# Kernel optimization log

Hardware: AMD Instinct MI355X
Metric: run time of the kernel (lower is better)

## Reference

```python
import jax, jax.numpy as jnp
import numpy as np

N = 100000   # nodes
E = 800000   # edges
G = 64       # graphs in batch
H_LSTM = 256


def setup_inputs() -> dict:
    key = jax.random.key(0)
    ks = jax.random.split(key, 24)

    def rn(k, shape, scale=0.05):
        return jax.random.normal(k, shape, dtype=jnp.float32) * scale

    inp = {
        "x": jax.random.normal(ks[0], (N, 32), dtype=jnp.float32),
        "edge_index": jax.random.randint(ks[1], (2, E), 0, N, dtype=jnp.int64),
        "batch_idx": jnp.sort(jax.random.randint(ks[2], (N,), 0, G, dtype=jnp.int64)),
        # GCN layer weights (in_dim x out_dim) + bias
        "W1": rn(ks[3], (32, 128)),   "b1": jnp.zeros((128,), jnp.float32),
        "W2": rn(ks[4], (128, 256)),  "b2": jnp.zeros((256,), jnp.float32),
        "W3": rn(ks[5], (256, 512)),  "b3": jnp.zeros((512,), jnp.float32),
        # LSTM layer 0: input 512 -> hidden 256, gates order (i,f,g,o)
        "Wih0": rn(ks[6], (4 * H_LSTM, 512)), "Whh0": rn(ks[7], (4 * H_LSTM, H_LSTM)),
        "bih0": jnp.zeros((4 * H_LSTM,), jnp.float32), "bhh0": jnp.zeros((4 * H_LSTM,), jnp.float32),
        # LSTM layer 1: input 256 -> hidden 256
        "Wih1": rn(ks[8], (4 * H_LSTM, H_LSTM)), "Whh1": rn(ks[9], (4 * H_LSTM, H_LSTM)),
        "bih1": jnp.zeros((4 * H_LSTM,), jnp.float32), "bhh1": jnp.zeros((4 * H_LSTM,), jnp.float32),
        # output projection 256 -> 512
        "Wp": rn(ks[10], (512, H_LSTM)), "bp": jnp.zeros((512,), jnp.float32),
    }
    return inp


def _lstm_cell(xt, Wih, Whh, bih, bhh):
    B = xt.shape[0]
    H = Whh.shape[1]
    h0 = jnp.zeros((B, H), xt.dtype)
    c0 = jnp.zeros((B, H), xt.dtype)
    gates = xt @ Wih.T + h0 @ Whh.T + bih + bhh  # [B, 4H]
    i = jax.nn.sigmoid(gates[:, 0 * H:1 * H])
    f = jax.nn.sigmoid(gates[:, 1 * H:2 * H])
    g = jnp.tanh(gates[:, 2 * H:3 * H])
    o = jax.nn.sigmoid(gates[:, 3 * H:4 * H])
    c = f * c0 + i * g
    return o * jnp.tanh(c)


def reference(x, edge_index, batch_idx, W1, b1, W2, b2, W3, b3,
              Wih0, Whh0, bih0, bhh0, Wih1, Whh1, bih1, bhh1, Wp, bp):
    src, dst = edge_index[0], edge_index[1]
    # symmetric GCN normalization with self-loops (PyG GCNConv default)
    deg = jax.ops.segment_sum(jnp.ones((E,), x.dtype), dst, num_segments=N) + 1.0
    dinv = jax.lax.rsqrt(deg)
    edge_norm = (dinv[src] * dinv[dst])[:, None]
    self_norm = (dinv * dinv)[:, None]

    def gcn(h, W, b):
        h = h @ W                                            # transform first (smaller gather)
        msg = h[src] * edge_norm                             # [E, out]
        agg = jax.ops.segment_sum(msg, dst, num_segments=N)  # scatter-add to targets
        agg = agg + h * self_norm                            # self-loop contribution
        return jax.nn.relu(agg + b)

    h = gcn(x, W1, b1)
    h = gcn(h, W2, b2)
    h = gcn(h, W3, b3)  # [N, 512]

    # global mean pool per graph
    counts = jax.ops.segment_sum(jnp.ones((N,), h.dtype), batch_idx, num_segments=G)
    pooled = jax.ops.segment_sum(h, batch_idx, num_segments=G) / jnp.maximum(counts, 1.0)[:, None]

    # 2-layer LSTM over seq_len=1 (zero initial state)
    h1 = _lstm_cell(pooled, Wih0, Whh0, bih0, bhh0)
    h2 = _lstm_cell(h1, Wih1, Whh1, bih1, bhh1)
    return h2 @ Wp.T + bp  # [G, 512]
```

## Files before the change

kernel.cpp:

```cpp
#include <hip/hip_runtime.h>
#include <math.h>
#include <type_traits>


__device__ __forceinline__ float bf2f(unsigned short u) {
    union { unsigned int i; float f; } v; v.i = ((unsigned int)u) << 16; return v.f;
}
__device__ __forceinline__ unsigned short f2bf(float f) {
    union { float f_; unsigned int i; } v; v.f_ = f;
    unsigned int x = v.i;
    return (unsigned short)((x + 0x7fffu + ((x >> 16) & 1u)) >> 16);
}
__device__ __forceinline__ float sigm(float x) { return 1.f / (1.f + expf(-x)); }

typedef __attribute__((ext_vector_type(8))) short short8;
typedef __attribute__((ext_vector_type(16))) float f32x16;


__global__ void k_init(int* __restrict__ indeg, int* __restrict__ cursor,
                       int* __restrict__ gstart, int* __restrict__ gend,
                       float* __restrict__ pooled, int N) {
    int i = blockIdx.x * 256 + threadIdx.x;
    if (i < N) indeg[i] = 0;
    else if (i < 2 * N) cursor[i - N] = 0;
    else if (i < 2 * N + 64) gstart[i - 2 * N] = 0;
    else if (i < 2 * N + 128) gend[i - 2 * N - 64] = 0;
    else if (i < 2 * N + 128 + 64 * 512) pooled[i - 2 * N - 128] = 0.f;
}


template <int K, int NC>
__device__ __forceinline__ void prep_elem(const float* __restrict__ W,
                                          unsigned short* __restrict__ Wf, int idx) {
    constexpr int S = K / 16;
    int lane = idx & 63;
    int ts = idx >> 6;
    int s = ts % S, t = ts / S;
    int n = t * 32 + (lane & 31);
    int kb = s * 16 + (lane >> 5) * 8;
    short8 o;
    #pragma unroll
    for (int j = 0; j < 8; ++j) o[j] = (short)f2bf(W[(size_t)(kb + j) * NC + n]);
    *(short8*)(Wf + (size_t)idx * 8) = o;
}

__global__ void k_count(const int* __restrict__ dst, int* __restrict__ indeg, int E,
                        const float* __restrict__ W1, unsigned short* __restrict__ Wf1,
                        const float* __restrict__ W2, unsigned short* __restrict__ Wf2,
                        const float* __restrict__ W3, unsigned short* __restrict__ Wf3) {
    constexpr int P1 = 32 * 128 / 8, P2 = 128 * 256 / 8, P3 = 256 * 512 / 8;
    int i = blockIdx.x * 256 + threadIdx.x;
    if (i < E) atomicAdd(&indeg[dst[i]], 1);
    if (i < P1) prep_elem<32, 128>(W1, Wf1, i);
    else if (i < P1 + P2) prep_elem<128, 256>(W2, Wf2, i - P1);
    else if (i < P1 + P2 + P3) prep_elem<256, 512>(W3, Wf3, i - P1 - P2);
}


__global__ __launch_bounds__(1024) void k_scan1(const int* __restrict__ in, int* __restrict__ out,
                                                int* __restrict__ bsum, float* __restrict__ dinv,
                                                const float* __restrict__ x, float* __restrict__ xs,
                                                int N) {
    __shared__ int sd[1024];
    __shared__ float sdv[1024];
    int tid = threadIdx.x;
    int i = blockIdx.x * 1024 + tid;
    int v = (i < N) ? in[i] : 0;
    float dv = rsqrtf((float)v + 1.0f);
    if (i < N) dinv[i] = dv;
    sdv[tid] = dv;
    sd[tid] = v;
    __syncthreads();
    for (int s = 1; s < 1024; s <<= 1) {
        int t = (tid >= s) ? sd[tid - s] : 0;
        __syncthreads();
        sd[tid] += t;
        __syncthreads();
    }
    if (i < N) out[i] = sd[tid] - v;
    if (tid == 1023) bsum[blockIdx.x] = sd[1023];
    int base = blockIdx.x * 1024;
    const float4* x4 = (const float4*)x;
    float4* xs4 = (float4*)xs;
    #pragma unroll
    for (int rep = 0; rep < 8; ++rep) {
        int j = rep * 1024 + tid;
        int node = base + (j >> 3);
        if (node < N) {
            float4 t = x4[(size_t)base * 8 + j];
            float s = sdv[j >> 3];
            t.x *= s; t.y *= s; t.z *= s; t.w *= s;
            xs4[(size_t)base * 8 + j] = t;
        }
    }
}

__global__ __launch_bounds__(256) void k_scan2(int* __restrict__ bsum, int nb) {
    __shared__ int sd[256];
    int tid = threadIdx.x;
    int v = (tid < nb) ? bsum[tid] : 0;
    sd[tid] = v;
    __syncthreads();
    for (int s = 1; s < 256; s <<= 1) {
        int t = (tid >= s) ? sd[tid - s] : 0;
        __syncthreads();
        sd[tid] += t;
        __syncthreads();
    }
    if (tid < nb) bsum[tid] = sd[tid] - v;
    if (tid == 0) bsum[nb] = sd[255];
}

__global__ __launch_bounds__(1024) void k_scan3(int* __restrict__ off, const int* __restrict__ bsum,
                                                const int* __restrict__ batch,
                                                int* __restrict__ gstart, int* __restrict__ gend,
                                                int N, int nb) {
    int i = blockIdx.x * 1024 + threadIdx.x;
    if (i < N) {
        off[i] += bsum[i >> 10];
        int g = batch[i];
        if (i == 0 || batch[i - 1] != g) gstart[g] = i;
        if (i == N - 1 || batch[i + 1] != g) gend[g] = i + 1;
    } else if (i == N) {
        off[N] = bsum[nb];
    }
}

__global__ void k_fill(const int* __restrict__ src, const int* __restrict__ dst,
                       const int* __restrict__ off, int* __restrict__ cursor,
                       int* __restrict__ csrc, int E) {
    int i = blockIdx.x * 256 + threadIdx.x;
    if (i >= E) return;
    int d = dst[i];
    int p = off[d] + atomicAdd(&cursor[d], 1);
    csrc[p] = src[i];
}


template <int F, typename T>
__device__ __forceinline__ void agg_body(
        const T* __restrict__ Hin, const float* __restrict__ dinv,
        const int* __restrict__ off, const int* __restrict__ csrc,
        unsigned short* __restrict__ out, int N) {
    constexpr int R = (F >= 256) ? 4 : (F >= 128 ? 2 : 1);
    int wave = (int)((blockIdx.x * 256u + threadIdx.x) >> 6);
    int lane = threadIdx.x & 63;
    if (wave >= N) return;
    int fb = (F >= 64) ? lane * R : lane;
    bool act = fb < F;
    int s0 = off[wave], s1 = off[wave + 1];
    int L = s1 - s0;
    float corr = 1.0f - (float)(((L + 7) & ~7) - L);
    float dn = dinv[wave];
    float acc[R];
    #pragma unroll
    for (int j = 0; j < R; ++j) acc[j] = 0.f;

    for (int e = s0; e < s1; e += 8) {
        int idx[8];
        #pragma unroll
        for (int j = 0; j < 8; ++j) {
            int ee = e + j;
            int ix = csrc[ee];
            idx[j] = (ee < s1) ? ix : wave;
        }
        if (act) {
            if constexpr (std::is_same_v<T, float>) {
                float d0[8];
                #pragma unroll
                for (int j = 0; j < 8; ++j) d0[j] = Hin[(size_t)idx[j] * F + fb];
                #pragma unroll
                for (int j = 0; j < 8; ++j) acc[0] += d0[j];
            } else if constexpr (R == 4) {
                ushort4 d0[8];
                #pragma unroll
                for (int j = 0; j < 8; ++j)
                    d0[j] = *(const ushort4*)(Hin + (size_t)idx[j] * F + fb);
                #pragma unroll
                for (int j = 0; j < 8; ++j) {
                    acc[0] += bf2f(d0[j].x); acc[1] += bf2f(d0[j].y);
                    acc[2] += bf2f(d0[j].z); acc[3] += bf2f(d0[j].w);
                }
            } else {
                ushort2 d0[8];
                #pragma unroll
                for (int j = 0; j < 8; ++j)
                    d0[j] = *(const ushort2*)(Hin + (size_t)idx[j] * F + fb);
                #pragma unroll
                for (int j = 0; j < 8; ++j) {
                    acc[0] += bf2f(d0[j].x); acc[1] += bf2f(d0[j].y);
                }
            }
        }
    }
    if (act) {
        const T* ps = Hin + (size_t)wave * F + fb;
        unsigned short* pd = out + (size_t)wave * F + fb;
        if constexpr (std::is_same_v<T, float>) {
            pd[0] = f2bf((acc[0] + corr * ps[0]) * dn);
        } else if constexpr (R == 4) {
            ushort4 hv = *(const ushort4*)ps;
            ushort4 o;
            o.x = f2bf((acc[0] + corr * bf2f(hv.x)) * dn);
            o.y = f2bf((acc[1] + corr * bf2f(hv.y)) * dn);
            o.z = f2bf((acc[2] + corr * bf2f(hv.z)) * dn);
            o.w = f2bf((acc[3] + corr * bf2f(hv.w)) * dn);
            *(ushort4*)pd = o;
        } else {
            ushort2 hv = *(const ushort2*)ps;
            ushort2 o;
            o.x = f2bf((acc[0] + corr * bf2f(hv.x)) * dn);
            o.y = f2bf((acc[1] + corr * bf2f(hv.y)) * dn);
            *(ushort2*)pd = o;
        }
    }
}

__global__ __launch_bounds__(256) void k_aggL1(
        const float* __restrict__ Hin, const float* __restrict__ dinv,
        const int* __restrict__ off, const int* __restrict__ csrc,
        unsigned short* __restrict__ out, int N) {
    agg_body<32, float>(Hin, dinv, off, csrc, out, N);
}

__global__ __launch_bounds__(256) void k_aggL2(
        const unsigned short* __restrict__ Hin, const float* __restrict__ dinv,
        const int* __restrict__ off, const int* __restrict__ csrc,
        unsigned short* __restrict__ out, int N) {
    agg_body<128, unsigned short>(Hin, dinv, off, csrc, out, N);
}

__global__ __launch_bounds__(256) void k_aggL3pair(
        const unsigned short* __restrict__ Hin, const float* __restrict__ dinv,
        const int* __restrict__ off, const int* __restrict__ csrc,
        unsigned short* __restrict__ out, int N) {
    constexpr int F = 256;
    int wave = (int)((blockIdx.x * 256u + threadIdx.x) >> 6);
    int lane = threadIdx.x & 63;
    if (wave >= N) return;
    int half = lane >> 5;
    int fb = (lane & 31) * 8;
    int s0 = off[wave], s1 = off[wave + 1];
    int L = s1 - s0;
    float corrTot = 1.0f - (float)(((L + 15) & ~15) - L);
    float acc[8];
    #pragma unroll
    for (int k = 0; k < 8; ++k) acc[k] = 0.f;

    for (int e = s0; e < s1; e += 16) {
        int idx[8];
        #pragma unroll
        for (int j = 0; j < 8; ++j) {
            int ee = e + j * 2 + half;
            int ix = csrc[ee];
            idx[j] = (ee < s1) ? ix : wave;
        }
        short8 d0[8];
        #pragma unroll
        for (int j = 0; j < 8; ++j)
            d0[j] = *(const short8*)(Hin + (size_t)idx[j] * F + fb);
        #pragma unroll
        for (int j = 0; j < 8; ++j) {
            #pragma unroll
            for (int k = 0; k < 8; ++k)
                acc[k] += bf2f((unsigned short)d0[j][k]);
        }
    }
    #pragma unroll
    for (int k = 0; k < 8; ++k) acc[k] += __shfl_xor(acc[k], 32, 64);

    if (half == 0) {
        float dn = dinv[wave];
        short8 selfv = *(const short8*)(Hin + (size_t)wave * F + fb);
        short8 o;
        #pragma unroll
        for (int k = 0; k < 8; ++k)
            o[k] = (short)f2bf((acc[k] + corrTot * bf2f((unsigned short)selfv[k])) * dn);
        *(short8*)(out + (size_t)wave * F + fb) = o;
    }
}


template <int K, int NC, int POOL>
__device__ __forceinline__ void gemm_body(
        const unsigned short* __restrict__ A, const unsigned short* __restrict__ Wf,
        const float* __restrict__ bias, const float* __restrict__ dinv,
        unsigned short* __restrict__ C,
        float* __restrict__ pooled, float* __restrict__ partial,
        int* __restrict__ gtile, const int* __restrict__ batch, int M) {
    constexpr int S = K / 16;
    constexpr int CPR = K / 8;
    constexpr int NT = NC / 32;
    __shared__ unsigned short sA[64 * K];
    __shared__ int sbat[POOL ? 64 : 1];
    __shared__ float sdv[POOL ? 1 : 64];
    int tid = threadIdx.x, lane = tid & 63, w = tid >> 6;
    int q = lane >> 5, m = lane & 31;
    int row0 = blockIdx.x * 64;

    if (tid < 64) {
        int rr = row0 + tid; if (rr > M - 1) rr = M - 1;
        if (POOL) sbat[tid] = batch[rr];
        else      sdv[tid] = dinv[rr];
    }

    #pragma unroll
    for (int i = 0; i < (64 * CPR) / 256; ++i) {
        int g = i * 256 + tid;
        int mm = g / CPR, kc = g % CPR;
        int grow = row0 + mm; if (grow > M - 1) grow = M - 1;
        short8 v = *(const short8*)(A + (size_t)grow * K + kc * 8);
        int xm = (CPR >= 8) ? (mm & 7) : ((mm >> 1) & 3);
        *(short8*)(sA + (size_t)(mm * CPR + (kc ^ xm)) * 8) = v;
    }
    __syncthreads();

    int gmin = 0; bool fast = false;
    unsigned int selMask = 0;
    if (POOL) {
        gmin = sbat[0];
        fast = (sbat[63] - gmin) <= 1;
        if (tid == 0) gtile[blockIdx.x] = gmin;
        #pragma unroll
        for (int half = 0; half < 2; ++half) {
            #pragma unroll
            for (int j = 0; j < 16; ++j) {
                int rloc = half * 32 + (j & 3) + 8 * (j >> 2) + 4 * q;
                if (sbat[rloc] != gmin) selMask |= 1u << (half * 16 + j);
            }
        }
    }

    const short8* Wf8 = (const short8*)Wf;
    for (int t = w; t < NT; t += 4) {
        short8 bF[S];
        #pragma unroll
        for (int s = 0; s < S; ++s) bF[s] = Wf8[(t * S + s) * 64 + lane];
        int colBase = t * 32 + m;
        float bv = bias[colBase];
        float p0 = 0.f, p1 = 0.f;
        #pragma unroll
        for (int half = 0; half < 2; ++half) {
            int mrow = half * 32 + m;
            int xm = (CPR >= 8) ? (mrow & 7) : ((mrow >> 1) & 3);
            f32x16 acc;
            #pragma unroll
            for (int j = 0; j < 16; ++j) acc[j] = 0.f;
            #pragma unroll
            for (int s = 0; s < S; ++s) {
                int kc = s * 2 + q;
                short8 aF = *(const short8*)(sA + (size_t)(mrow * CPR + (kc ^ xm)) * 8);
                acc = __builtin_amdgcn_mfma_f32_32x32x16_bf16(aF, bF[s], acc, 0, 0, 0);
            }
            #pragma unroll
            for (int j = 0; j < 16; ++j) {
                int rloc = half * 32 + (j & 3) + 8 * (j >> 2) + 4 * q;
                int row = row0 + rloc;
                if (row < M) {
                    float v = fmaxf(acc[j] + bv, 0.f);
                    if (POOL) {
                        if (fast) {
                            bool sel = (selMask >> (half * 16 + j)) & 1u;
                            p0 += sel ? 0.f : v;
                            p1 += sel ? v : 0.f;
                        } else {
                            atomicAdd(&pooled[(size_t)sbat[rloc] * NC + colBase], v);
                        }
                    } else {
                        C[(size_t)row * NC + colBase] = f2bf(v * sdv[rloc]);
                    }
                }
            }
        }
        if (POOL) {
            p0 += __shfl_xor(p0, 32, 64);
            p1 += __shfl_xor(p1, 32, 64);
            if (q == 0) {
                partial[((size_t)blockIdx.x * 2 + 0) * NC + colBase] = p0;
                partial[((size_t)blockIdx.x * 2 + 1) * NC + colBase] = p1;
            }
        }
    }
}

__global__ __launch_bounds__(256, 2) void k_gemmL1(
        const unsigned short* __restrict__ A, const unsigned short* __restrict__ Wf,
        const float* __restrict__ bias, const float* __restrict__ dinv,
        unsigned short* __restrict__ C, int M) {
    gemm_body<32, 128, 0>(A, Wf, bias, dinv, C, nullptr, nullptr, nullptr, nullptr, M);
}

__global__ __launch_bounds__(256, 2) void k_gemmL2(
        const unsigned short* __restrict__ A, const unsigned short* __restrict__ Wf,
        const float* __restrict__ bias, const float* __restrict__ dinv,
        unsigned short* __restrict__ C, int M) {
    gemm_body<128, 256, 0>(A, Wf, bias, dinv, C, nullptr, nullptr, nullptr, nullptr, M);
}

__global__ __launch_bounds__(256, 2) void k_gemmL3pool(
        const unsigned short* __restrict__ A, const unsigned short* __restrict__ Wf,
        const float* __restrict__ bias, float* __restrict__ pooled,
        float* __restrict__ partial, int* __restrict__ gtile,
        const int* __restrict__ batch, int M) {
    gemm_body<256, 512, 1>(A, Wf, bias, nullptr, nullptr, pooled, partial, gtile, batch, M);
}


__global__ __launch_bounds__(256) void k_pool(
        const float* __restrict__ pooled, const float* __restrict__ partial,
        const int* __restrict__ gtile,
        const int* __restrict__ gstart, const int* __restrict__ gend,
        float* __restrict__ xmean) {
    int g = blockIdx.x, tid = threadIdx.x;
    int gs = gstart[g], ge = gend[g];
    float inv = 1.f / fmaxf((float)(ge - gs), 1.f);
    float a0 = pooled[g * 512 + tid];
    float a1 = pooled[g * 512 + 256 + tid];
    if (ge > gs) {
        int t0 = gs >> 6, t1 = (ge - 1) >> 6;
        for (int t = t0; t <= t1; ++t) {
            unsigned int slot = (unsigned int)(g - gtile[t]);
            if (slot < 2u) {
                const float* p = partial + ((size_t)t * 2 + slot) * 512;
                a0 += p[tid];
                a1 += p[tid + 256];
            }
        }
    }
    xmean[g * 512 + tid]       = a0 * inv;
    xmean[g * 512 + 256 + tid] = a1 * inv;
}

__device__ __forceinline__ float dot8(const float* __restrict__ w,
                                      float4 x0, float4 x1) {
    float4 a = *(const float4*)w, b = *(const float4*)(w + 4);
    return a.x * x0.x + a.y * x0.y + a.z * x0.z + a.w * x0.w +
           b.x * x1.x + b.y * x1.y + b.z * x1.z + b.w * x1.w;
}
__device__ __forceinline__ float dot4(const float* __restrict__ w, float4 x) {
    float4 a = *(const float4*)w;
    return a.x * x.x + a.y * x.y + a.z * x.z + a.w * x.w;
}

__global__ __launch_bounds__(256) void k_lstm0(
        const float* __restrict__ xmean, const float* __restrict__ Wih0,
        const float* __restrict__ bih0, const float* __restrict__ bhh0,
        float* __restrict__ h1) {
    int wid = (int)((blockIdx.x * 256u + threadIdx.x) >> 6);
    int lane = threadIdx.x & 63;
    int g = wid >> 8, hu = wid & 255;
    int k0 = lane * 8;
    const float* xp = xmean + g * 512 + k0;
    float4 x0 = *(const float4*)xp, x1 = *(const float4*)(xp + 4);
    float ai = dot8(Wih0 + (size_t)hu * 512 + k0, x0, x1);
    float ag = dot8(Wih0 + (size_t)(hu + 512) * 512 + k0, x0, x1);
    float ao = dot8(Wih0 + (size_t)(hu + 768) * 512 + k0, x0, x1);
    #pragma unroll
    for (int msk = 32; msk >= 1; msk >>= 1) {
        ai += __shfl_xor(ai, msk, 64);
        ag += __shfl_xor(ag, msk, 64);
        ao += __shfl_xor(ao, msk, 64);
    }
    if (lane == 0) {
        ai += bih0[hu]       + bhh0[hu];
        ag += bih0[hu + 512] + bhh0[hu + 512];
        ao += bih0[hu + 768] + bhh0[hu + 768];
        float c0 = sigm(ai) * tanhf(ag);
        h1[g * 256 + hu] = sigm(ao) * tanhf(c0);
    }
}

__global__ __launch_bounds__(256) void k_lstm1(
        const float* __restrict__ h1, const float* __restrict__ Wih1,
        const float* __restrict__ bih1, const float* __restrict__ bhh1,
        float* __restrict__ h2) {
    int wid = (int)((blockIdx.x * 256u + threadIdx.x) >> 6);
    int lane = threadIdx.x & 63;
    int g = wid >> 8, hu = wid & 255;
    int k0 = lane * 4;
    float4 x = *(const float4*)(h1 + g * 256 + k0);
    float ai = dot4(Wih1 + (size_t)hu * 256 + k0, x);
    float ag = dot4(Wih1 + (size_t)(hu + 512) * 256 + k0, x);
    float ao = dot4(Wih1 + (size_t)(hu + 768) * 256 + k0, x);
    #pragma unroll
    for (int msk = 32; msk >= 1; msk >>= 1) {
        ai += __shfl_xor(ai, msk, 64);
        ag += __shfl_xor(ag, msk, 64);
        ao += __shfl_xor(ao, msk, 64);
    }
    if (lane == 0) {
        ai += bih1[hu]       + bhh1[hu];
        ag += bih1[hu + 512] + bhh1[hu + 512];
        ao += bih1[hu + 768] + bhh1[hu + 768];
        float c1 = sigm(ai) * tanhf(ag);
        h2[g * 256 + hu] = sigm(ao) * tanhf(c1);
    }
}

__global__ __launch_bounds__(256) void k_out(
        const float* __restrict__ h2, const float* __restrict__ Wp,
        const float* __restrict__ bp, float* __restrict__ out) {
    int wid = (int)((blockIdx.x * 256u + threadIdx.x) >> 6);
    int lane = threadIdx.x & 63;
    int g = wid >> 9, r = wid & 511;
    int k0 = lane * 4;
    float4 x = *(const float4*)(h2 + g * 256 + k0);
    float a = dot4(Wp + (size_t)r * 256 + k0, x);
    #pragma unroll
    for (int msk = 32; msk >= 1; msk >>= 1) a += __shfl_xor(a, msk, 64);
    if (lane == 0) out[g * 512 + r] = a + bp[r];
}


extern "C" void kernel_launch(void* const* d_in, const int* in_sizes, int n_in,
                              void* d_out, int out_size, void* d_ws, size_t ws_size,
                              hipStream_t stream) {
    const float* x     = (const float*)d_in[0];
    const int*   eidx  = (const int*)d_in[1];
    const int*   batch = (const int*)d_in[2];
    const float* W1 = (const float*)d_in[3];  const float* b1 = (const float*)d_in[4];
    const float* W2 = (const float*)d_in[5];  const float* b2 = (const float*)d_in[6];
    const float* W3 = (const float*)d_in[7];  const float* b3 = (const float*)d_in[8];
    const float* Wih0 = (const float*)d_in[9];
    const float* bih0 = (const float*)d_in[11];
    const float* bhh0 = (const float*)d_in[12];
    const float* Wih1 = (const float*)d_in[13];
    const float* bih1 = (const float*)d_in[15];
    const float* bhh1 = (const float*)d_in[16];
    const float* Wp = (const float*)d_in[17]; const float* bp = (const float*)d_in[18];
    float* out = (float*)d_out;

    const int N = in_sizes[0] / 32;
    const int E = in_sizes[1] / 2;
    const int* src = eidx;
    const int* dst = eidx + E;
    const int rowTiles = (N + 63) / 64;

    char* w = (char*)d_ws;
    auto alloc = [&](size_t bytes) {
        char* p = w;
        w += (bytes + 255) & ~(size_t)255;
        return p;
    };
    unsigned short* buf1 = (unsigned short*)alloc((size_t)N * 256 * 2);
    unsigned short* buf2 = (unsigned short*)alloc((size_t)N * 256 * 2);
    unsigned short* Wf1  = (unsigned short*)alloc(128 * 32 * 2);
    unsigned short* Wf2  = (unsigned short*)alloc(256 * 128 * 2);
    unsigned short* Wf3  = (unsigned short*)alloc(512 * 256 * 2);
    int*   indeg  = (int*)alloc((size_t)N * 4);
    int*   off    = (int*)alloc((size_t)(N + 1) * 4);
    int*   cursor = (int*)alloc((size_t)N * 4);
    float* dinv   = (float*)alloc((size_t)N * 4);
    int*   csrc   = (int*)alloc((size_t)(E + 64) * 4);
    float* xs     = (float*)alloc((size_t)N * 32 * 4);
    int*   bsum   = (int*)alloc(8192);
    int*   gstart = (int*)alloc(64 * 4);
    int*   gend   = (int*)alloc(64 * 4);
    float* pooled = (float*)alloc(64 * 512 * 4);
    float* xmean  = (float*)alloc(64 * 512 * 4);
    float* h1buf  = (float*)alloc(64 * 256 * 4);
    float* h2buf  = (float*)alloc(64 * 256 * 4);

    float* partial = xs;
    int*   gtile   = cursor;

    int initTot = 2 * N + 128 + 64 * 512;
    k_init<<<(initTot + 255) / 256, 256, 0, stream>>>(indeg, cursor, gstart, gend, pooled, N);
    k_count<<<(E + 255) / 256, 256, 0, stream>>>(dst, indeg, E, W1, Wf1, W2, Wf2, W3, Wf3);
    int nb = (N + 1023) / 1024;
    k_scan1<<<nb, 1024, 0, stream>>>(indeg, off, bsum, dinv, x, xs, N);
    k_scan2<<<1, 256, 0, stream>>>(bsum, nb);
    k_scan3<<<(N + 1 + 1023) / 1024, 1024, 0, stream>>>(off, bsum, batch, gstart, gend, N, nb);
    k_fill<<<(E + 255) / 256, 256, 0, stream>>>(src, dst, off, cursor, csrc, E);

    int aggBlocks = (N + 3) / 4;

    k_aggL1<<<aggBlocks, 256, 0, stream>>>(xs, dinv, off, csrc, buf1, N);
    k_gemmL1<<<rowTiles, 256, 0, stream>>>(buf1, Wf1, b1, dinv, buf2, N);
    k_aggL2<<<aggBlocks, 256, 0, stream>>>(buf2, dinv, off, csrc, buf1, N);
    k_gemmL2<<<rowTiles, 256, 0, stream>>>(buf1, Wf2, b2, dinv, buf2, N);
    k_aggL3pair<<<aggBlocks, 256, 0, stream>>>(buf2, dinv, off, csrc, buf1, N);
    k_gemmL3pool<<<rowTiles, 256, 0, stream>>>(buf1, Wf3, b3, pooled, partial, gtile, batch, N);

    k_pool<<<64, 256, 0, stream>>>(pooled, partial, gtile, gstart, gend, xmean);
    k_lstm0<<<4096, 256, 0, stream>>>(xmean, Wih0, bih0, bhh0, h1buf);
    k_lstm1<<<4096, 256, 0, stream>>>(h1buf, Wih1, bih1, bhh1, h2buf);
    k_out<<<8192, 256, 0, stream>>>(h2buf, Wp, bp, out);
}
```

Measured before the change: 457.5 us.

## Store scaled input in bf16 and restructure aggregation kernels for full lane use

The prescaled input features are now stored as bf16 instead of fp32, which halves gather traffic in the first aggregation. The layer-1 and layer-2 aggregation kernels are rewritten so that all 64 lanes are active. Lanes are split into edge groups with vectorized loads and combined by shuffle reductions, instead of leaving most lanes idle. Outputs use nontemporal stores and the wave index is made uniform with readfirstlane. The cost is extra bf16 rounding of the inputs. The xs buffer is enlarged so it can still hold the aliased partial-sum buffer.

```diff
diff --git a/kernel.cpp b/kernel.cpp
--- a/kernel.cpp
+++ b/kernel.cpp
@@ -15,6 +15,12 @@
 
 typedef __attribute__((ext_vector_type(8))) short short8;
 typedef __attribute__((ext_vector_type(16))) float f32x16;
+
+__device__ __forceinline__ void nt_store8(unsigned short* p, ushort4 o) {
+    unsigned long long ob;
+    __builtin_memcpy(&ob, &o, 8);
+    __builtin_nontemporal_store(ob, (unsigned long long*)p);
+}
 
 
 __global__ void k_init(int* __restrict__ indeg, int* __restrict__ cursor,
@@ -59,7 +65,8 @@
 
 __global__ __launch_bounds__(1024) void k_scan1(const int* __restrict__ in, int* __restrict__ out,
                                                 int* __restrict__ bsum, float* __restrict__ dinv,
-                                                const float* __restrict__ x, float* __restrict__ xs,
+                                                const float* __restrict__ x,
+                                                unsigned short* __restrict__ xs,
                                                 int N) {
     __shared__ int sd[1024];
     __shared__ float sdv[1024];
@@ -81,7 +88,7 @@
     if (tid == 1023) bsum[blockIdx.x] = sd[1023];
     int base = blockIdx.x * 1024;
     const float4* x4 = (const float4*)x;
-    float4* xs4 = (float4*)xs;
+    ushort4* xs4 = (ushort4*)xs;
     #pragma unroll
     for (int rep = 0; rep < 8; ++rep) {
         int j = rep * 1024 + tid;
@@ -89,8 +96,10 @@
         if (node < N) {
             float4 t = x4[(size_t)base * 8 + j];
             float s = sdv[j >> 3];
-            t.x *= s; t.y *= s; t.z *= s; t.w *= s;
-            xs4[(size_t)base * 8 + j] = t;
+            ushort4 o;
+            o.x = f2bf(t.x * s); o.y = f2bf(t.y * s);
+            o.z = f2bf(t.z * s); o.w = f2bf(t.w * s);
+            xs4[(size_t)base * 8 + j] = o;
         }
     }
 }
@@ -137,97 +146,95 @@
 }
 
 
-template <int F, typename T>
-__device__ __forceinline__ void agg_body(
-        const T* __restrict__ Hin, const float* __restrict__ dinv,
+__global__ __launch_bounds__(256) void k_aggL1(
+        const unsigned short* __restrict__ Hin, const float* __restrict__ dinv,
         const int* __restrict__ off, const int* __restrict__ csrc,
         unsigned short* __restrict__ out, int N) {
-    constexpr int R = (F >= 256) ? 4 : (F >= 128 ? 2 : 1);
-    int wave = (int)((blockIdx.x * 256u + threadIdx.x) >> 6);
+    constexpr int F = 32;
+    int wv = __builtin_amdgcn_readfirstlane(
+        (int)((blockIdx.x * 256u + threadIdx.x) >> 6));
+    if (wv >= N) return;
     int lane = threadIdx.x & 63;
-    if (wave >= N) return;
-    int fb = (F >= 64) ? lane * R : lane;
-    bool act = fb < F;
-    int s0 = off[wave], s1 = off[wave + 1];
+    int grp = lane >> 3;
+    int cl = (lane & 7) * 4;
+    int s0 = off[wv], s1 = off[wv + 1];
     int L = s1 - s0;
     float corr = 1.0f - (float)(((L + 7) & ~7) - L);
-    float dn = dinv[wave];
-    float acc[R];
-    #pragma unroll
-    for (int j = 0; j < R; ++j) acc[j] = 0.f;
-
+    float dn = dinv[wv];
+    float acc[4] = {0.f, 0.f, 0.f, 0.f};
     for (int e = s0; e < s1; e += 8) {
-        int idx[8];
-        #pragma unroll
-        for (int j = 0; j < 8; ++j) {
-            int ee = e + j;
-            int ix = csrc[ee];
-            idx[j] = (ee < s1) ? ix : wave;
-        }
-        if (act) {
-            if constexpr (std::is_same_v<T, float>) {
-                float d0[8];
-                #pragma unroll
-                for (int j = 0; j < 8; ++j) d0[j] = Hin[(size_t)idx[j] * F + fb];
-                #pragma unroll
-                for (int j = 0; j < 8; ++j) acc[0] += d0[j];
-            } else if constexpr (R == 4) {
-                ushort4 d0[8];
-                #pragma unroll
-                for (int j = 0; j < 8; ++j)
-                    d0[j] = *(const ushort4*)(Hin + (size_t)idx[j] * F + fb);
-                #pragma unroll
-                for (int j = 0; j < 8; ++j) {
-                    acc[0] += bf2f(d0[j].x); acc[1] += bf2f(d0[j].y);
-                    acc[2] += bf2f(d0[j].z); acc[3] += bf2f(d0[j].w);
-                }
-            } else {
-                ushort2 d0[8];
-                #pragma unroll
-                for (int j = 0; j < 8; ++j)
-                    d0[j] = *(const ushort2*)(Hin + (size_t)idx[j] * F + fb);
-                #pragma unroll
-                for (int j = 0; j < 8; ++j) {
-                    acc[0] += bf2f(d0[j].x); acc[1] += bf2f(d0[j].y);
-                }
-            }
-        }
-    }
-    if (act) {
-        const T* ps = Hin + (size_t)wave * F + fb;
-        unsigned short* pd = out + (size_t)wave * F + fb;
-        if constexpr (std::is_same_v<T, float>) {
-            pd[0] = f2bf((acc[0] + corr * ps[0]) * dn);
-        } else if constexpr (R == 4) {
-            ushort4 hv = *(const ushort4*)ps;
-            ushort4 o;
-            o.x = f2bf((acc[0] + corr * bf2f(hv.x)) * dn);
-            o.y = f2bf((acc[1] + corr * bf2f(hv.y)) * dn);
-            o.z = f2bf((acc[2] + corr * bf2f(hv.z)) * dn);
-            o.w = f2bf((acc[3] + corr * bf2f(hv.w)) * dn);
-            *(ushort4*)pd = o;
-        } else {
-            ushort2 hv = *(const ushort2*)ps;
-            ushort2 o;
-            o.x = f2bf((acc[0] + corr * bf2f(hv.x)) * dn);
-            o.y = f2bf((acc[1] + corr * bf2f(hv.y)) * dn);
-            *(ushort2*)pd = o;
-        }
-    }
-}
-
-__global__ __launch_bounds__(256) void k_aggL1(
-        const float* __restrict__ Hin, const float* __restrict__ dinv,
-        const int* __restrict__ off, const int* __restrict__ csrc,
-        unsigned short* __restrict__ out, int N) {
-    agg_body<32, float>(Hin, dinv, off, csrc, out, N);
+        int ee = e + grp;
+        int ix = csrc[ee];
+        int idx = (ee < s1) ? ix : wv;
+        ushort4 v = *(const ushort4*)(Hin + (size_t)idx * F + cl);
+        acc[0] += bf2f(v.x); acc[1] += bf2f(v.y);
+        acc[2] += bf2f(v.z); acc[3] += bf2f(v.w);
+    }
+    #pragma unroll
+    for (int msk = 8; msk <= 32; msk <<= 1) {
+        acc[0] += __shfl_xor(acc[0], msk, 64);
+        acc[1] += __shfl_xor(acc[1], msk, 64);
+        acc[2] += __shfl_xor(acc[2], msk, 64);
+        acc[3] += __shfl_xor(acc[3], msk, 64);
+    }
+    if (grp == 0) {
+        ushort4 sv = *(const ushort4*)(Hin + (size_t)wv * F + cl);
+        ushort4 o;
+        o.x = f2bf((acc[0] + corr * bf2f(sv.x)) * dn);
+        o.y = f2bf((acc[1] + corr * bf2f(sv.y)) * dn);
+        o.z = f2bf((acc[2] + corr * bf2f(sv.z)) * dn);
+        o.w = f2bf((acc[3] + corr * bf2f(sv.w)) * dn);
+        nt_store8(out + (size_t)wv * F + cl, o);
+    }
 }
 
 __global__ __launch_bounds__(256) void k_aggL2(
         const unsigned short* __restrict__ Hin, const float* __restrict__ dinv,
         const int* __restrict__ off, const int* __restrict__ csrc,
         unsigned short* __restrict__ out, int N) {
-    agg_body<128, unsigned short>(Hin, dinv, off, csrc, out, N);
+    constexpr int F = 128;
+    int wv = __builtin_amdgcn_readfirstlane(
+        (int)((blockIdx.x * 256u + threadIdx.x) >> 6));
+    if (wv >= N) return;
+    int lane = threadIdx.x & 63;
+    int half = lane >> 5;
+    int fb = (lane & 31) * 4;
+    int s0 = off[wv], s1 = off[wv + 1];
+    int L = s1 - s0;
+    float corrTot = 1.0f - (float)(((L + 15) & ~15) - L);
+    float acc[4] = {0.f, 0.f, 0.f, 0.f};
+
+    for (int e = s0; e < s1; e += 16) {
+        int idx[8];
+        #pragma unroll
+        for (int j = 0; j < 8; ++j) {
+            int ee = e + j * 2 + half;
+            int ix = csrc[ee];
+            idx[j] = (ee < s1) ? ix : wv;
+        }
+        ushort4 d0[8];
+        #pragma unroll
+        for (int j = 0; j < 8; ++j)
+            d0[j] = *(const ushort4*)(Hin + (size_t)idx[j] * F + fb);
+        #pragma unroll
+        for (int j = 0; j < 8; ++j) {
+            acc[0] += bf2f(d0[j].x); acc[1] += bf2f(d0[j].y);
+            acc[2] += bf2f(d0[j].z); acc[3] += bf2f(d0[j].w);
+        }
+    }
+    #pragma unroll
+    for (int k = 0; k < 4; ++k) acc[k] += __shfl_xor(acc[k], 32, 64);
+
+    if (half == 0) {
+        float dn = dinv[wv];
+        ushort4 sv = *(const ushort4*)(Hin + (size_t)wv * F + fb);
+        ushort4 o;
+        o.x = f2bf((acc[0] + corrTot * bf2f(sv.x)) * dn);
+        o.y = f2bf((acc[1] + corrTot * bf2f(sv.y)) * dn);
+        o.z = f2bf((acc[2] + corrTot * bf2f(sv.z)) * dn);
+        o.w = f2bf((acc[3] + corrTot * bf2f(sv.w)) * dn);
+        nt_store8(out + (size_t)wv * F + fb, o);
+    }
 }
 
 __global__ __launch_bounds__(256) void k_aggL3pair(
@@ -235,12 +242,13 @@
         const int* __restrict__ off, const int* __restrict__ csrc,
         unsigned short* __restrict__ out, int N) {
     constexpr int F = 256;
-    int wave = (int)((blockIdx.x * 256u + threadIdx.x) >> 6);
+    int wv = __builtin_amdgcn_readfirstlane(
+        (int)((blockIdx.x * 256u + threadIdx.x) >> 6));
+    if (wv >= N) return;
     int lane = threadIdx.x & 63;
-    if (wave >= N) return;
     int half = lane >> 5;
     int fb = (lane & 31) * 8;
-    int s0 = off[wave], s1 = off[wave + 1];
+    int s0 = off[wv], s1 = off[wv + 1];
     int L = s1 - s0;
     float corrTot = 1.0f - (float)(((L + 15) & ~15) - L);
     float acc[8];
@@ -253,7 +261,7 @@
         for (int j = 0; j < 8; ++j) {
             int ee = e + j * 2 + half;
             int ix = csrc[ee];
-            idx[j] = (ee < s1) ? ix : wave;
+            idx[j] = (ee < s1) ? ix : wv;
         }
         short8 d0[8];
         #pragma unroll
@@ -270,13 +278,13 @@
     for (int k = 0; k < 8; ++k) acc[k] += __shfl_xor(acc[k], 32, 64);
 
     if (half == 0) {
-        float dn = dinv[wave];
-        short8 selfv = *(const short8*)(Hin + (size_t)wave * F + fb);
+        float dn = dinv[wv];
+        short8 selfv = *(const short8*)(Hin + (size_t)wv * F + fb);
         short8 o;
         #pragma unroll
         for (int k = 0; k < 8; ++k)
             o[k] = (short)f2bf((acc[k] + corrTot * bf2f((unsigned short)selfv[k])) * dn);
-        *(short8*)(out + (size_t)wave * F + fb) = o;
+        __builtin_nontemporal_store(o, (short8*)(out + (size_t)wv * F + fb));
     }
 }
 
@@ -552,7 +560,7 @@
     int*   cursor = (int*)alloc((size_t)N * 4);
     float* dinv   = (float*)alloc((size_t)N * 4);
     int*   csrc   = (int*)alloc((size_t)(E + 64) * 4);
-    float* xs     = (float*)alloc((size_t)N * 32 * 4);
+    unsigned short* xs = (unsigned short*)alloc((size_t)N * 32 * 2 + 65536);
     int*   bsum   = (int*)alloc(8192);
     int*   gstart = (int*)alloc(64 * 4);
     int*   gend   = (int*)alloc(64 * 4);
@@ -561,7 +569,7 @@
     float* h1buf  = (float*)alloc(64 * 256 * 4);
     float* h2buf  = (float*)alloc(64 * 256 * 4);
 
-    float* partial = xs;
+    float* partial = (float*)xs;
     int*   gtile   = cursor;
 
     int initTot = 2 * N + 128 + 64 * 512;
```

Result: faster. 447.2 us (-2.3%).
